# Kernel tuning notes

Hardware: AMD Instinct MI355X
Metric: run time of the kernel (lower is better)

## Reference

```python
import jax, jax.numpy as jnp
import numpy as np
from jax import lax

DIM = 1024
INNER = 2048          # expansion * dim
GROUPS = 128          # groups in cell's 1x1 grouped convs
GSZ = INNER // GROUPS # 16
KSZ = 4               # causal conv kernel size
EPS = 1e-8


def log_g(x):
    return jnp.where(x >= 0, jnp.log(jax.nn.relu(x) + 0.5 + EPS), -jax.nn.softplus(-x) + EPS)


def setup_inputs() -> dict:
    key = jax.random.key(0)
    ks = jax.random.split(key, 10)
    B, S = 4, 4096
    std_up = float(np.sqrt(2.0 / (5 * DIM)))
    std_down = float(2.0 / 1 / np.sqrt(DIM))
    return {
        "x": jax.random.normal(ks[0], (B, S, DIM), jnp.float32),
        "w_up": jax.random.normal(ks[1], (2 * INNER, DIM), jnp.float32) * std_up,
        "b_up": jnp.zeros((2 * INNER,), jnp.float32),
        "conv_w": jax.random.normal(ks[2], (INNER, 1, KSZ), jnp.float32) * 0.25,
        "conv_b": jnp.zeros((INNER,), jnp.float32),
        "skip": jnp.ones((INNER,), jnp.float32),
        "w_f": jax.random.normal(ks[3], (GROUPS, GSZ, GSZ), jnp.float32) * 0.1,
        "w_i": jax.random.normal(ks[4], (GROUPS, GSZ, GSZ), jnp.float32) * 0.1,
        "w_h": jax.random.normal(ks[5], (GROUPS, GSZ, GSZ), jnp.float32) * 0.1,
        "w_down": jax.random.normal(ks[6], (DIM, INNER), jnp.float32) * std_down,
        "b_down": jnp.zeros((DIM,), jnp.float32),
    }


def reference(x, w_up, b_up, conv_w, conv_b, skip, w_f, w_i, w_h, w_down, b_down):
    B, S, _ = x.shape
    # proj up -> split into minlstm branch and gate branch z
    x_inner = jnp.einsum('bsd,ed->bse', x, w_up) + b_up          # (B,S,2*INNER)
    x_min, z = jnp.split(x_inner, 2, axis=-1)                    # each (B,S,INNER)

    # causal depthwise conv over time (left pad K-1, cross-correlation like torch)
    xc = lax.conv_general_dilated(
        x_min.transpose(0, 2, 1), conv_w,
        window_strides=(1,), padding=[(KSZ - 1, 0)],
        feature_group_count=INNER,
        dimension_numbers=('NCH', 'OIH', 'NCH'))
    xc = (xc + conv_b[None, :, None]).transpose(0, 2, 1)         # (B,S,INNER)
    act = jax.nn.silu(xc)

    # minLSTM cell: grouped (block-diagonal, 128 blocks of 16) 1x1 projections
    ag = act.reshape(B, S, GROUPS, GSZ)
    f_gate = jnp.einsum('bsgi,goi->bsgo', ag, w_f).reshape(B, S, INNER)
    i_gate = jnp.einsum('bsgi,goi->bsgo', ag, w_i).reshape(B, S, INNER)
    hidden = jnp.einsum('bsgi,goi->bsgo', ag, w_h).reshape(B, S, INNER)

    diff = jax.nn.softplus(-f_gate) - jax.nn.softplus(-i_gate)
    log_f = -jax.nn.softplus(diff)
    log_i = -jax.nn.softplus(-diff)
    log_tilde_h = log_g(hidden)

    # parallel log-space scan
    a_star = jnp.cumsum(log_f + EPS, axis=1)
    log_h0_b = lax.cumlogsumexp(log_i + log_tilde_h - a_star, axis=1)
    h_t = jnp.exp(a_star + log_h0_b)                             # (B,S,INNER)

    # original code keeps only last timestep of the scan, broadcast over skip path
    h = h_t[:, -1:, :] + skip * act                              # (B,S,INNER)
    h = h * jax.nn.silu(z)
    out = jnp.einsum('bse,de->bsd', h, w_down) + b_down          # (B,S,DIM)
    return out
```

## Files before the change

kernel.cpp:

```cpp
#include <hip/hip_runtime.h>
#include <math.h>

constexpr int B_  = 4;
constexpr int S_  = 4096;
constexpr int D_  = 1024;
constexpr int IN_ = 2048;
constexpr float EPS_ = 1e-8f;
constexpr int NCH_ = 128;
constexpr int CS_  = S_ / NCH_;
constexpr float LOG2E_ = 1.4426950408889634f;
constexpr float LN2_   = 0.6931471805599453f;

typedef __attribute__((ext_vector_type(8))) _Float16 f16x8;
typedef __attribute__((ext_vector_type(2))) _Float16 h2;
typedef __attribute__((ext_vector_type(4))) float    f32x4;

#define BAR() asm volatile("s_barrier" ::: "memory")

__device__ __forceinline__ h2 pkrtz(float a, float b) {
  auto r = __builtin_amdgcn_cvt_pkrtz(a, b);
  union { decltype(r) r_; h2 h; } c; c.r_ = r; return c.h;
}
__device__ __forceinline__ unsigned packh2(float a, float b) {
  auto r = __builtin_amdgcn_cvt_pkrtz(a, b);
  union { decltype(r) r_; unsigned u; } c; c.r_ = r; return c.u;
}
__device__ __forceinline__ void unpack_h8(uint4 v, float* f) {
  union { uint4 u; _Float16 h[8]; } c; c.u = v;
  #pragma unroll
  for (int i = 0; i < 8; ++i) f[i] = (float)c.h[i];
}
__device__ __forceinline__ float spf_fast(float t) {
  const float e = __builtin_amdgcn_exp2f(-fabsf(t) * LOG2E_);
  return fmaxf(t, 0.0f) + LN2_ * __builtin_amdgcn_logf(1.0f + e);
}
__device__ __forceinline__ float siluf(float x) {
  return x * __builtin_amdgcn_rcpf(1.0f + __builtin_amdgcn_exp2f(-x * LOG2E_));
}

__device__ __forceinline__ void gload16(const void* g, void* l) {
  __builtin_amdgcn_global_load_lds(
      (const __attribute__((address_space(1))) void*)g,
      (__attribute__((address_space(3))) void*)l,
      16, 0, 0);
}

__launch_bounds__(256)
__global__ void cvt_f16(const float* __restrict__ in, unsigned* __restrict__ outp,
                        long n8)
{
  const long stride = (long)gridDim.x * blockDim.x;
  for (long i = (long)blockIdx.x * blockDim.x + threadIdx.x; i < n8; i += stride) {
    const float4 a = *(const float4*)(in + i * 8);
    const float4 b = *(const float4*)(in + i * 8 + 4);
    uint4 o;
    o.x = packh2(a.x, a.y);
    o.y = packh2(a.z, a.w);
    o.z = packh2(b.x, b.y);
    o.w = packh2(b.z, b.w);
    *(uint4*)(outp + i * 4) = o;
  }
}

template<int MODE>
__launch_bounds__(512, 2)
__global__ void gemm_mfma(const unsigned short* __restrict__ Ab,
                          const unsigned short* __restrict__ Bb,
                          const float* __restrict__ bias,
                          void* __restrict__ out0,
                          unsigned short* __restrict__ out1,
                          int M, int N, int K)
{
  constexpr int BM = 256, BN = 256, BK = 64;
  __shared__ __align__(16) unsigned short As[2][BM * BK];
  __shared__ __align__(16) unsigned short Bs[2][BN * BK];

  const int tid  = threadIdx.x;
  const int lane = tid & 63;
  const int w    = tid >> 6;
  const int wm   = w >> 2;
  const int wn   = w & 3;

  const int GX  = gridDim.x;
  const int nwg = GX * gridDim.y;
  int lin = blockIdx.y * GX + blockIdx.x;
  lin = (lin & 7) * (nwg >> 3) + (lin >> 3);
  const int m0 = (lin / GX) * BM;
  const int n0 = (lin % GX) * BN;
  const int NT = K / BK;

  const int sr   = lane >> 3;
  const int sblk = ((lane & 7) ^ sr) * 8;

  const int fr  = lane & 15;
  const int fb0 = (((lane >> 4) + 0) ^ (lane & 7)) * 8;
  const int fb1 = (((lane >> 4) + 4) ^ (lane & 7)) * 8;

  auto stage64 = [&](const unsigned short* Gp, int Kd, int grow0, int kOff,
                     unsigned short* lchunk) {
    gload16(Gp + (size_t)(grow0 + w * 8 + sr) * Kd + kOff + sblk,
            lchunk + (w * 8) * BK);
  };

  f32x4 acc[8][4] = {};

  #pragma unroll
  for (int c = 0; c < 4; ++c) stage64(Ab, K, m0 + c * 64, 0, &As[0][c * 64 * BK]);
  #pragma unroll
  for (int c = 0; c < 4; ++c) stage64(Bb, K, n0 + c * 64, 0, &Bs[0][c * 64 * BK]);
  #pragma unroll
  for (int c = 0; c < 4; ++c) stage64(Ab, K, m0 + c * 64, BK, &As[1][c * 64 * BK]);
  #pragma unroll
  for (int c = 0; c < 4; ++c) stage64(Bb, K, n0 + c * 64, BK, &Bs[1][c * 64 * BK]);
  asm volatile("s_waitcnt vmcnt(8)" ::: "memory");
  BAR();

  for (int t = 0; t < NT; ++t) {
    const int cur = t & 1;
    const unsigned short* AL = As[cur];
    const unsigned short* BL = Bs[cur];
    const int  nxtK = (t + 2) * BK;
    const bool more = (t + 2 < NT);

    f16x8 af[4][2], bf[4][2];

    #pragma unroll
    for (int i = 0; i < 4; ++i) {
      const int row = wm * 128 + i * 16 + fr;
      af[i][0] = *(const f16x8*)&AL[row * BK + fb0];
      af[i][1] = *(const f16x8*)&AL[row * BK + fb1];
    }
    #pragma unroll
    for (int j = 0; j < 2; ++j) {
      const int row = wn * 64 + j * 16 + fr;
      bf[j][0] = *(const f16x8*)&BL[row * BK + fb0];
      bf[j][1] = *(const f16x8*)&BL[row * BK + fb1];
    }
    BAR();
    __builtin_amdgcn_s_setprio(1);
    #pragma unroll
    for (int i = 0; i < 4; ++i)
      #pragma unroll
      for (int j = 0; j < 2; ++j) {
        acc[i][j] = __builtin_amdgcn_mfma_f32_16x16x32_f16(af[i][0], bf[j][0], acc[i][j], 0, 0, 0);
        acc[i][j] = __builtin_amdgcn_mfma_f32_16x16x32_f16(af[i][1], bf[j][1], acc[i][j], 0, 0, 0);
      }
    __builtin_amdgcn_s_setprio(0);
    BAR();

    #pragma unroll
    for (int j = 2; j < 4; ++j) {
      const int row = wn * 64 + j * 16 + fr;
      bf[j][0] = *(const f16x8*)&BL[row * BK + fb0];
      bf[j][1] = *(const f16x8*)&BL[row * BK + fb1];
    }
    BAR();
    __builtin_amdgcn_s_setprio(1);
    #pragma unroll
    for (int i = 0; i < 4; ++i)
      #pragma unroll
      for (int j = 2; j < 4; ++j) {
        acc[i][j] = __builtin_amdgcn_mfma_f32_16x16x32_f16(af[i][0], bf[j][0], acc[i][j], 0, 0, 0);
        acc[i][j] = __builtin_amdgcn_mfma_f32_16x16x32_f16(af[i][1], bf[j][1], acc[i][j], 0, 0, 0);
      }
    __builtin_amdgcn_s_setprio(0);
    BAR();

    #pragma unroll
    for (int i = 0; i < 4; ++i) {
      const int row = wm * 128 + 64 + i * 16 + fr;
      af[i][0] = *(const f16x8*)&AL[row * BK + fb0];
      af[i][1] = *(const f16x8*)&AL[row * BK + fb1];
    }
    if (more) {
      stage64(Bb, K, n0 +   0, nxtK, &Bs[cur][0]);
      stage64(Bb, K, n0 +  64, nxtK, &Bs[cur][64 * BK]);
      stage64(Ab, K, m0 +   0, nxtK, &As[cur][0]);
      stage64(Ab, K, m0 + 128, nxtK, &As[cur][128 * BK]);
    }
    BAR();
    __builtin_amdgcn_s_setprio(1);
    #pragma unroll
    for (int i = 0; i < 4; ++i)
      #pragma unroll
      for (int j = 0; j < 2; ++j) {
        acc[4 + i][j] = __builtin_amdgcn_mfma_f32_16x16x32_f16(af[i][0], bf[j][0], acc[4 + i][j], 0, 0, 0);
        acc[4 + i][j] = __builtin_amdgcn_mfma_f32_16x16x32_f16(af[i][1], bf[j][1], acc[4 + i][j], 0, 0, 0);
      }
    __builtin_amdgcn_s_setprio(0);
    BAR();

    if (more) {
      stage64(Bb, K, n0 + 128, nxtK, &Bs[cur][128 * BK]);
      stage64(Bb, K, n0 + 192, nxtK, &Bs[cur][192 * BK]);
      stage64(Ab, K, m0 +  64, nxtK, &As[cur][64 * BK]);
      stage64(Ab, K, m0 + 192, nxtK, &As[cur][192 * BK]);
    }
    BAR();
    __builtin_amdgcn_s_setprio(1);
    #pragma unroll
    for (int i = 0; i < 4; ++i)
      #pragma unroll
      for (int j = 2; j < 4; ++j) {
        acc[4 + i][j] = __builtin_amdgcn_mfma_f32_16x16x32_f16(af[i][0], bf[j][0], acc[4 + i][j], 0, 0, 0);
        acc[4 + i][j] = __builtin_amdgcn_mfma_f32_16x16x32_f16(af[i][1], bf[j][1], acc[4 + i][j], 0, 0, 0);
      }
    __builtin_amdgcn_s_setprio(0);
    if (more) asm volatile("s_waitcnt vmcnt(8)" ::: "memory");
    else      asm volatile("s_waitcnt vmcnt(0)" ::: "memory");
    BAR();
  }

  const int col = lane & 15;
  const int rb4 = (lane >> 4) * 4;

  if (MODE == 1) {
    #pragma unroll
    for (int j = 0; j < 4; ++j) {
      const int n  = n0 + wn * 64 + j * 16 + col;
      const float bv = bias[n];
      #pragma unroll
      for (int i = 0; i < 8; ++i) {
        const int mb = m0 + wm * 128 + i * 16 + rb4;
        #pragma unroll
        for (int r = 0; r < 4; ++r)
          ((float*)out0)[(size_t)(mb + r) * N + n] = acc[i][j][r] + bv;
      }
    }
  } else {
    constexpr int RS = 72;
    unsigned short* eb = (w < 4) ? ((unsigned short*)As + w * (64 * RS))
                                 : ((unsigned short*)Bs + (w - 4) * (64 * RS));
    const bool zhalf = (n0 >= IN_);
    float bv[4];
    #pragma unroll
    for (int j = 0; j < 4; ++j) bv[j] = bias[n0 + wn * 64 + j * 16 + col];

    const int lrow = lane >> 3;
    const int lc8  = (lane & 7) * 8;
    unsigned short* dst = zhalf ? out1 : (unsigned short*)out0;
    const int ncol0 = (zhalf ? n0 - IN_ : n0) + wn * 64 + lc8;

    #pragma unroll
    for (int h = 0; h < 2; ++h) {
      asm volatile("s_waitcnt lgkmcnt(0)" ::: "memory");
      #pragma unroll
      for (int i2 = 0; i2 < 4; ++i2)
        #pragma unroll
        for (int j = 0; j < 4; ++j)
          #pragma unroll
          for (int r = 0; r < 4; ++r) {
            const float v = acc[h * 4 + i2][j][r] + bv[j];
            ((_Float16*)eb)[(i2 * 16 + rb4 + r) * RS + j * 16 + col] = (_Float16)v;
          }
      asm volatile("s_waitcnt lgkmcnt(0)" ::: "memory");
      #pragma unroll
      for (int it = 0; it < 8; ++it) {
        const int row = it * 8 + lrow;
        uint4 d = *(const uint4*)&eb[row * RS + lc8];
        if (zhalf) {
          float f[8];
          unpack_h8(d, f);
          d.x = packh2(siluf(f[0]), siluf(f[1]));
          d.y = packh2(siluf(f[2]), siluf(f[3]));
          d.z = packh2(siluf(f[4]), siluf(f[5]));
          d.w = packh2(siluf(f[6]), siluf(f[7]));
        }
        const int m = m0 + wm * 128 + h * 64 + row;
        *(uint4*)(dst + (size_t)m * IN_ + ncol0) = d;
      }
    }
  }
}

__launch_bounds__(256)
__global__ void conv_silu_k(const uint4* __restrict__ xm,
                            const float* __restrict__ cw,
                            const float* __restrict__ cb,
                            uint4* __restrict__ act)
{
  const int t = blockIdx.x * 256 + threadIdx.x;
  const int c8 = t & 255;
  const int s4 = (t >> 8) & (S_ / 4 - 1);
  const int b  = t >> 18;
  const int c  = c8 * 8;
  constexpr int RW = IN_ / 8;

  float w[8][4];
  #pragma unroll
  for (int j = 0; j < 8; ++j)
    *(float4*)w[j] = *(const float4*)(cw + (size_t)(c + j) * 4);
  float bias8[8];
  *(float4*)(bias8)     = *(const float4*)(cb + c);
  *(float4*)(bias8 + 4) = *(const float4*)(cb + c + 4);

  const size_t rowb = ((size_t)b * S_ + s4 * 4) * RW + c8;
  float xf[7][8];
  #pragma unroll
  for (int i = 0; i < 7; ++i) {
    const int srow = s4 * 4 - 3 + i;
    if (s4 == 0 && i < 3) {
      #pragma unroll
      for (int j = 0; j < 8; ++j) xf[i][j] = 0.0f;
    } else {
      unpack_h8(xm[rowb + (long)(i - 3) * RW], xf[i]);
    }
  }

  #pragma unroll
  for (int o = 0; o < 4; ++o) {
    float r[8];
    #pragma unroll
    for (int j = 0; j < 8; ++j) r[j] = bias8[j];
    #pragma unroll
    for (int k = 0; k < 4; ++k)
      #pragma unroll
      for (int j = 0; j < 8; ++j)
        r[j] = fmaf(xf[o + k][j], w[j][k], r[j]);
    uint4 ov;
    ov.x = packh2(siluf(r[0]), siluf(r[1]));
    ov.y = packh2(siluf(r[2]), siluf(r[3]));
    ov.z = packh2(siluf(r[4]), siluf(r[5]));
    ov.w = packh2(siluf(r[6]), siluf(r[7]));
    act[rowb + (size_t)o * RW] = ov;
  }
}

__launch_bounds__(256)
__global__ void gates_scan(const unsigned* __restrict__ actb,
                           const float* __restrict__ wf,
                           const float* __restrict__ wi,
                           const float* __restrict__ wh,
                           float2* __restrict__ part)
{
  const int T  = blockIdx.x * 256 + threadIdx.x;
  const int o  = T & 15;
  const int g  = (T >> 4) & 127;
  const int ck = (T >> 11) & (NCH_ - 1);
  const int b  = T >> 18;

  h2 Wf2[8], Wi2[8], Wh2[8];
  const float* pf = wf + ((size_t)g * 16 + o) * 16;
  const float* pi = wi + ((size_t)g * 16 + o) * 16;
  const float* ph = wh + ((size_t)g * 16 + o) * 16;
  #pragma unroll
  for (int i = 0; i < 8; ++i) {
    Wf2[i] = pkrtz(pf[2 * i], pf[2 * i + 1]);
    Wi2[i] = pkrtz(pi[2 * i], pi[2 * i + 1]);
    Wh2[i] = pkrtz(ph[2 * i], ph[2 * i + 1]);
  }

  float p = 0.0f, Mx = -INFINITY, Ss = 0.0f;
  const unsigned* ap = actb + ((size_t)b * S_ + (size_t)ck * CS_) * (IN_ / 2) + g * 8;
  for (int s = 0; s < CS_; ++s) {
    union { uint4 u; h2 h[4]; } A0, A1;
    A0.u = *(const uint4*)(ap);
    A1.u = *(const uint4*)(ap + 4);
    ap += IN_ / 2;
    float fg = 0.0f, ig = 0.0f, hd = 0.0f;
    #pragma unroll
    for (int i = 0; i < 4; ++i) {
      fg = __builtin_amdgcn_fdot2(A0.h[i], Wf2[i], fg, false);
      ig = __builtin_amdgcn_fdot2(A0.h[i], Wi2[i], ig, false);
      hd = __builtin_amdgcn_fdot2(A0.h[i], Wh2[i], hd, false);
    }
    #pragma unroll
    for (int i = 0; i < 4; ++i) {
      fg = __builtin_amdgcn_fdot2(A1.h[i], Wf2[i + 4], fg, false);
      ig = __builtin_amdgcn_fdot2(A1.h[i], Wi2[i + 4], ig, false);
      hd = __builtin_amdgcn_fdot2(A1.h[i], Wh2[i + 4], hd, false);
    }
    const float diff  = spf_fast(-fg) - spf_fast(-ig);
    const float log_f = -spf_fast(diff);
    const float log_i = diff + log_f;
    const float lpos  = LN2_ * __builtin_amdgcn_logf(hd + 0.5f + EPS_);
    const float lneg  = -spf_fast(-hd) + EPS_;
    const float log_th = (hd >= 0.0f) ? lpos : lneg;
    p += log_f + EPS_;
    const float v = log_i + log_th - p;
    const float m = fmaxf(Mx, v);
    Ss = Ss * __builtin_amdgcn_exp2f((Mx - m) * LOG2E_)
       + __builtin_amdgcn_exp2f((v - m) * LOG2E_);
    Mx = m;
  }
  part[((size_t)(b * IN_ + g * 16 + o)) * NCH_ + ck] =
      make_float2(p, Mx + LN2_ * __builtin_amdgcn_logf(Ss));
}

__launch_bounds__(256)
__global__ void combine_k(const float2* __restrict__ part, float* __restrict__ hlast)
{
  const int seq = blockIdx.x * 256 + threadIdx.x;
  if (seq >= B_ * IN_) return;
  const float2* pp = part + (size_t)seq * NCH_;
  float P = 0.0f, Mx = -INFINITY, Ss = 0.0f;
  for (int c = 0; c < NCH_; ++c) {
    const float2 al = pp[c];
    const float v = al.y - P;
    const float m = fmaxf(Mx, v);
    Ss = Ss * __builtin_amdgcn_exp2f((Mx - m) * LOG2E_)
       + __builtin_amdgcn_exp2f((v - m) * LOG2E_);
    Mx = m;
    P += al.x;
  }
  hlast[seq] = __builtin_amdgcn_exp2f((P + Mx) * LOG2E_) * Ss;
}

__launch_bounds__(256)
__global__ void gfuse_k(const unsigned* __restrict__ actb,
                        unsigned* __restrict__ zb,
                        const float* __restrict__ hlast,
                        const float* __restrict__ skipv)
{
  const size_t total  = (size_t)B_ * S_ * IN_ / 8;
  const size_t stride = (size_t)gridDim.x * blockDim.x;
  for (size_t t = (size_t)blockIdx.x * blockDim.x + threadIdx.x; t < total; t += stride) {
    const size_t e = t * 8;
    const int    c = (int)(e % IN_);
    const int    b = (int)(e / ((size_t)S_ * IN_));
    float a[8], z[8], hl[8], sk[8];
    unpack_h8(*(const uint4*)(actb + e / 2), a);
    unpack_h8(*(const uint4*)(zb   + e / 2), z);
    *(float4*)(hl)     = *(const float4*)(hlast + (size_t)b * IN_ + c);
    *(float4*)(hl + 4) = *(const float4*)(hlast + (size_t)b * IN_ + c + 4);
    *(float4*)(sk)     = *(const float4*)(skipv + c);
    *(float4*)(sk + 4) = *(const float4*)(skipv + c + 4);
    float g[8];
    #pragma unroll
    for (int j = 0; j < 8; ++j) g[j] = (hl[j] + sk[j] * a[j]) * z[j];
    uint4 o;
    o.x = packh2(g[0], g[1]);
    o.y = packh2(g[2], g[3]);
    o.z = packh2(g[4], g[5]);
    o.w = packh2(g[6], g[7]);
    *(uint4*)(zb + e / 2) = o;
  }
}

extern "C" void kernel_launch(void* const* d_in, const int* in_sizes, int n_in,
                              void* d_out, int out_size, void* d_ws, size_t ws_size,
                              hipStream_t stream)
{
  const float* x     = (const float*)d_in[0];
  const float* w_up  = (const float*)d_in[1];
  const float* b_up  = (const float*)d_in[2];
  const float* cw    = (const float*)d_in[3];
  const float* cb    = (const float*)d_in[4];
  const float* skipv = (const float*)d_in[5];
  const float* w_f   = (const float*)d_in[6];
  const float* w_i   = (const float*)d_in[7];
  const float* w_h   = (const float*)d_in[8];
  const float* w_dn  = (const float*)d_in[9];
  const float* b_dn  = (const float*)d_in[10];
  float* out = (float*)d_out;

  char* ws = (char*)d_ws;
  unsigned short* xminb = (unsigned short*)(ws);
  unsigned short* wdb   = (unsigned short*)(ws);
  float2*         part  = (float2*)(ws + 8388608ULL);
  float*          hlast = (float*)(ws + 16777216ULL);
  unsigned short* zb    = (unsigned short*)(ws + 67108864ULL);
  unsigned short* actb  = (unsigned short*)(ws + 134217728ULL);
  unsigned short* xb    = (unsigned short*)(ws + 134217728ULL);
  unsigned short* wub   = (unsigned short*)(ws + 201326592ULL);

  const int M = B_ * S_;

  cvt_f16<<<2048, 256, 0, stream>>>(x,    (unsigned*)xb,  (long)M * D_ / 8);
  cvt_f16<<<512,  256, 0, stream>>>(w_up, (unsigned*)wub, (long)2 * IN_ * D_ / 8);

  gemm_mfma<0><<<dim3((2 * IN_) / 256, M / 256), 512, 0, stream>>>(
      xb, wub, b_up, xminb, (unsigned short*)zb, M, 2 * IN_, D_);

  conv_silu_k<<<(B_ * (S_ / 4) * (IN_ / 8)) / 256, 256, 0, stream>>>(
      (const uint4*)xminb, cw, cb, (uint4*)actb);

  cvt_f16<<<256, 256, 0, stream>>>(w_dn, (unsigned*)wdb, (long)D_ * IN_ / 8);

  gates_scan<<<(B_ * 128 * 16 * NCH_) / 256, 256, 0, stream>>>(
      (const unsigned*)actb, w_f, w_i, w_h, part);

  combine_k<<<(B_ * IN_ + 255) / 256, 256, 0, stream>>>(part, hlast);

  gfuse_k<<<2048, 256, 0, stream>>>((const unsigned*)actb, (unsigned*)zb, hlast, skipv);

  gemm_mfma<1><<<dim3(D_ / 256, M / 256), 512, 0, stream>>>(
      zb, wdb, b_dn, out, nullptr, M, D_, IN_);
}
```

Before: 409.6 us.

## Move scan to base-2 log domain, fuse input casts, reorder GEMM staging

The gate and scan math now works in log2 units. The f and i gate weights are prescaled by log2(e), which drops the per-element LOG2E multiplies around exp2 and log2 in gates_scan and combine_k. The two fp32-to-fp16 conversion launches are merged into one kernel, saving a launch. In the GEMM main loop, the A-tile prefetch loads are issued earlier and spread across the phases to overlap better with MFMA work. The base-2 rescaling changes rounding slightly, and the EPS constant is rescaled to match.

```diff
diff --git a/kernel.cpp b/kernel.cpp
--- a/kernel.cpp
+++ b/kernel.cpp
@@ -10,6 +10,7 @@
 constexpr int CS_  = S_ / NCH_;
 constexpr float LOG2E_ = 1.4426950408889634f;
 constexpr float LN2_   = 0.6931471805599453f;
+constexpr float EPS2_  = 1.4426950408889634e-8f;
 
 typedef __attribute__((ext_vector_type(8))) _Float16 f16x8;
 typedef __attribute__((ext_vector_type(2))) _Float16 h2;
@@ -30,9 +31,9 @@
   #pragma unroll
   for (int i = 0; i < 8; ++i) f[i] = (float)c.h[i];
 }
-__device__ __forceinline__ float spf_fast(float t) {
-  const float e = __builtin_amdgcn_exp2f(-fabsf(t) * LOG2E_);
-  return fmaxf(t, 0.0f) + LN2_ * __builtin_amdgcn_logf(1.0f + e);
+__device__ __forceinline__ float sp2(float t) {
+  const float e = __builtin_amdgcn_exp2f(-fabsf(t));
+  return fmaxf(t, 0.0f) + __builtin_amdgcn_logf(1.0f + e);
 }
 __device__ __forceinline__ float siluf(float x) {
   return x * __builtin_amdgcn_rcpf(1.0f + __builtin_amdgcn_exp2f(-x * LOG2E_));
@@ -43,6 +44,29 @@
       (const __attribute__((address_space(1))) void*)g,
       (__attribute__((address_space(3))) void*)l,
       16, 0, 0);
+}
+
+__launch_bounds__(256)
+__global__ void cvt_f16_2(const float* __restrict__ in0, unsigned* __restrict__ out0,
+                          long n8_0,
+                          const float* __restrict__ in1, unsigned* __restrict__ out1,
+                          long n8_1)
+{
+  const long total  = n8_0 + n8_1;
+  const long stride = (long)gridDim.x * blockDim.x;
+  for (long t = (long)blockIdx.x * blockDim.x + threadIdx.x; t < total; t += stride) {
+    const float* in  = (t < n8_0) ? in0  : in1;
+    unsigned*    out = (t < n8_0) ? out0 : out1;
+    const long   i   = (t < n8_0) ? t    : t - n8_0;
+    const float4 a = *(const float4*)(in + i * 8);
+    const float4 b = *(const float4*)(in + i * 8 + 4);
+    uint4 o;
+    o.x = packh2(a.x, a.y);
+    o.y = packh2(a.z, a.w);
+    o.z = packh2(b.x, b.y);
+    o.w = packh2(b.z, b.w);
+    *(uint4*)(out + i * 4) = o;
+  }
 }
 
 __launch_bounds__(256)
@@ -154,6 +178,10 @@
       bf[j][0] = *(const f16x8*)&BL[row * BK + fb0];
       bf[j][1] = *(const f16x8*)&BL[row * BK + fb1];
     }
+    if (more) {
+      stage64(Ab, K, m0 +   0, nxtK, &As[cur][0]);
+      stage64(Ab, K, m0 + 128, nxtK, &As[cur][128 * BK]);
+    }
     BAR();
     __builtin_amdgcn_s_setprio(1);
     #pragma unroll
@@ -175,8 +203,6 @@
     if (more) {
       stage64(Bb, K, n0 +   0, nxtK, &Bs[cur][0]);
       stage64(Bb, K, n0 +  64, nxtK, &Bs[cur][64 * BK]);
-      stage64(Ab, K, m0 +   0, nxtK, &As[cur][0]);
-      stage64(Ab, K, m0 + 128, nxtK, &As[cur][128 * BK]);
     }
     BAR();
     __builtin_amdgcn_s_setprio(1);
@@ -191,10 +217,10 @@
     BAR();
 
     if (more) {
+      stage64(Ab, K, m0 +  64, nxtK, &As[cur][64 * BK]);
+      stage64(Ab, K, m0 + 192, nxtK, &As[cur][192 * BK]);
       stage64(Bb, K, n0 + 128, nxtK, &Bs[cur][128 * BK]);
       stage64(Bb, K, n0 + 192, nxtK, &Bs[cur][192 * BK]);
-      stage64(Ab, K, m0 +  64, nxtK, &As[cur][64 * BK]);
-      stage64(Ab, K, m0 + 192, nxtK, &As[cur][192 * BK]);
     }
     BAR();
     __builtin_amdgcn_s_setprio(1);
@@ -298,7 +324,6 @@
   float xf[7][8];
   #pragma unroll
   for (int i = 0; i < 7; ++i) {
-    const int srow = s4 * 4 - 3 + i;
     if (s4 == 0 && i < 3) {
       #pragma unroll
       for (int j = 0; j < 8; ++j) xf[i][j] = 0.0f;
@@ -345,8 +370,8 @@
   const float* ph = wh + ((size_t)g * 16 + o) * 16;
   #pragma unroll
   for (int i = 0; i < 8; ++i) {
-    Wf2[i] = pkrtz(pf[2 * i], pf[2 * i + 1]);
-    Wi2[i] = pkrtz(pi[2 * i], pi[2 * i + 1]);
+    Wf2[i] = pkrtz(pf[2 * i] * LOG2E_, pf[2 * i + 1] * LOG2E_);
+    Wi2[i] = pkrtz(pi[2 * i] * LOG2E_, pi[2 * i + 1] * LOG2E_);
     Wh2[i] = pkrtz(ph[2 * i], ph[2 * i + 1]);
   }
 
@@ -370,21 +395,20 @@
       ig = __builtin_amdgcn_fdot2(A1.h[i], Wi2[i + 4], ig, false);
       hd = __builtin_amdgcn_fdot2(A1.h[i], Wh2[i + 4], hd, false);
     }
-    const float diff  = spf_fast(-fg) - spf_fast(-ig);
-    const float log_f = -spf_fast(diff);
+    const float diff  = sp2(-fg) - sp2(-ig);
+    const float log_f = -sp2(diff);
     const float log_i = diff + log_f;
-    const float lpos  = LN2_ * __builtin_amdgcn_logf(hd + 0.5f + EPS_);
-    const float lneg  = -spf_fast(-hd) + EPS_;
+    const float lpos  = __builtin_amdgcn_logf(hd + 0.5f + EPS_);
+    const float lneg  = -sp2(-hd * LOG2E_) + EPS2_;
     const float log_th = (hd >= 0.0f) ? lpos : lneg;
-    p += log_f + EPS_;
+    p += log_f + EPS2_;
     const float v = log_i + log_th - p;
     const float m = fmaxf(Mx, v);
-    Ss = Ss * __builtin_amdgcn_exp2f((Mx - m) * LOG2E_)
-       + __builtin_amdgcn_exp2f((v - m) * LOG2E_);
+    Ss = Ss * __builtin_amdgcn_exp2f(Mx - m) + __builtin_amdgcn_exp2f(v - m);
     Mx = m;
   }
   part[((size_t)(b * IN_ + g * 16 + o)) * NCH_ + ck] =
-      make_float2(p, Mx + LN2_ * __builtin_amdgcn_logf(Ss));
+      make_float2(p, Mx + __builtin_amdgcn_logf(Ss));
 }
 
 __launch_bounds__(256)
@@ -398,12 +422,11 @@
     const float2 al = pp[c];
     const float v = al.y - P;
     const float m = fmaxf(Mx, v);
-    Ss = Ss * __builtin_amdgcn_exp2f((Mx - m) * LOG2E_)
-       + __builtin_amdgcn_exp2f((v - m) * LOG2E_);
+    Ss = Ss * __builtin_amdgcn_exp2f(Mx - m) + __builtin_amdgcn_exp2f(v - m);
     Mx = m;
     P += al.x;
   }
-  hlast[seq] = __builtin_amdgcn_exp2f((P + Mx) * LOG2E_) * Ss;
+  hlast[seq] = __builtin_amdgcn_exp2f(P + Mx) * Ss;
 }
 
 __launch_bounds__(256)
@@ -466,8 +489,9 @@
 
   const int M = B_ * S_;
 
-  cvt_f16<<<2048, 256, 0, stream>>>(x,    (unsigned*)xb,  (long)M * D_ / 8);
-  cvt_f16<<<512,  256, 0, stream>>>(w_up, (unsigned*)wub, (long)2 * IN_ * D_ / 8);
+  cvt_f16_2<<<2560, 256, 0, stream>>>(
+      x,    (unsigned*)xb,  (long)M * D_ / 8,
+      w_up, (unsigned*)wub, (long)2 * IN_ * D_ / 8);
 
   gemm_mfma<0><<<dim3((2 * IN_) / 256, M / 256), 512, 0, stream>>>(
       xb, wub, b_up, xminb, (unsigned short*)zb, M, 2 * IN_, D_);
```

Result: faster. 398.1 us (-2.8%).
